# Kernel tuning notes

Hardware: AMD Instinct MI355X
Metric: run time of the kernel (lower is better)

Reference implementation:

```python
import jax, jax.numpy as jnp
import numpy as np

B, V, D, H, ET = 32, 50, 6, 256, 4  # batch, num_vars, input_size, decoder_hidden, num_edge_types
E = V * (V - 1)                      # fully connected, no self-loops


def setup_inputs() -> dict:
    key = jax.random.key(0)
    ks = jax.random.split(key, 24)
    s = 0.05
    n = lambda k, shape: jax.random.normal(k, shape, jnp.float32)
    return {
        "inputs": n(ks[0], (B, V, D)),
        "hidden": n(ks[1], (B, V, H)),
        "edges": jax.random.uniform(ks[2], (B, E, ET), jnp.float32),
        # stacked per-edge-type message MLPs for the non-skipped types 1..ET-1
        "W1": n(ks[3], (ET - 1, H, 2 * H)) * s, "b1": jnp.full((ET - 1, H), 0.1, jnp.float32),
        "W2": n(ks[4], (ET - 1, H, H)) * s, "b2": jnp.full((ET - 1, H), 0.1, jnp.float32),
        # GRU-style update (hidden_* have no bias in the torch module)
        "Whr": n(ks[5], (H, H)) * s, "Whi": n(ks[6], (H, H)) * s, "Whh": n(ks[7], (H, H)) * s,
        "Wir": n(ks[8], (H, D)) * s, "bir": jnp.full((H,), 0.1, jnp.float32),
        "Wii": n(ks[9], (H, D)) * s, "bii": jnp.full((H,), 0.1, jnp.float32),
        "Win": n(ks[10], (H, D)) * s, "bin_w": jnp.full((H,), 0.1, jnp.float32),
        # output MLP
        "Wo1": n(ks[11], (H, H)) * s, "bo1": jnp.full((H,), 0.1, jnp.float32),
        "Wo2": n(ks[12], (H, H)) * s, "bo2": jnp.full((H,), 0.1, jnp.float32),
        "Wo3": n(ks[13], (D, H)) * s, "bo3": jnp.full((D,), 0.1, jnp.float32),
    }


def _edge_index(num_vars):
    mask = np.ones((num_vars, num_vars)) - np.eye(num_vars)
    send, recv = np.where(mask)
    onehot = np.zeros((send.shape[0], num_vars), dtype=np.float32)
    onehot[np.arange(send.shape[0]), recv] = 1.0  # edge2node scatter matrix [E, V]
    return send, recv, onehot


def reference(inputs, hidden, edges, W1, b1, W2, b2, Whr, Whi, Whh,
              Wir, bir, Wii, bii, Win, bin_w, Wo1, bo1, Wo2, bo2, Wo3, bo3):
    num_vars = hidden.shape[1]
    send, recv, onehot = _edge_index(num_vars)
    onehot = jnp.asarray(onehot)

    # gather: [B, E, 2H]
    pre_msg = jnp.concatenate([hidden[:, recv, :], hidden[:, send, :]], axis=-1)

    # per-edge-type message MLP (dropout is identity in eval mode), types 1..ET-1 (skip_first)
    m = jnp.tanh(jnp.einsum('bef,thf->bteh', pre_msg, W1) + b1[None, :, None, :])
    m = jnp.tanh(jnp.einsum('bteh,tgh->bteg', m, W2) + b2[None, :, None, :])
    ew = jnp.moveaxis(edges[:, :, 1:], -1, 1)          # [B, T, E]
    norm = edges.shape[-1] - 1
    all_msgs = jnp.einsum('bteh,bte->beh', m, ew) / norm  # [B, E, H]

    # scatter-aggregate edges -> receiver nodes
    agg = jnp.einsum('beh,ev->bvh', all_msgs, onehot) / (num_vars - 1)  # [B, V, H]

    # GRU-style gated update
    r = jax.nn.sigmoid(inputs @ Wir.T + bir + agg @ Whr.T)
    i = jax.nn.sigmoid(inputs @ Wii.T + bii + agg @ Whi.T)
    n_ = jnp.tanh(inputs @ Win.T + bin_w + r * (agg @ Whh.T))
    hidden_new = (1 - i) * n_ + i * hidden

    # output MLP with residual on inputs
    p = jax.nn.relu(hidden_new @ Wo1.T + bo1)
    p = jax.nn.relu(p @ Wo2.T + bo2)
    pred = inputs + (p @ Wo3.T + bo3)
    return pred, hidden_new
```

## Files before the change

kernel.cpp:

```cpp
#include <hip/hip_runtime.h>
#include <math.h>

#define B_ 32
#define V_ 50
#define D_ 6
#define H_ 256
#define E_ 2450
#define T_ 3
#define NN 1600

#define OFF_inputs 0
#define OFF_hidden 9600
#define OFF_edges  419200
#define OFF_W1     732800
#define OFF_b1     1126016
#define OFF_W2     1126784
#define OFF_b2     1323392
#define OFF_Whr    1324160
#define OFF_Whi    1389696
#define OFF_Whh    1455232
#define OFF_Wir    1520768
#define OFF_bir    1522304
#define OFF_Wii    1522560
#define OFF_bii    1524096
#define OFF_Win    1524352
#define OFF_binw   1525888
#define OFF_Wo1    1526144
#define OFF_bo1    1591680
#define OFF_Wo2    1591936
#define OFF_bo2    1657472
#define OFF_Wo3    1657728
#define OFF_bo3    1659264
#define TOTAL_IN   1659270

#define PW_W2   0
#define PW_W1   196608
#define PW_WG   589824
#define PW_WO1  786432
#define PW_WO2  851968
#define PW_HID  917504
#define PW_TOT  1327104

typedef __attribute__((ext_vector_type(8))) short short8;
typedef __attribute__((ext_vector_type(4))) float f32x4;

__device__ __forceinline__ float bfc(unsigned int u) {
    return __uint_as_float((u & 0xffffu) << 16);
}
__device__ __forceinline__ unsigned short f2bf(float f) {
    unsigned int x = __float_as_uint(f);
    unsigned int r = (x + 0x7fffu + ((x >> 16) & 1u)) >> 16;
    return (unsigned short)r;
}
__device__ __forceinline__ float tanh_fast(float x) {
    float e = __builtin_amdgcn_exp2f(x * 2.8853900817779268f);
    return 1.0f - 2.0f * __builtin_amdgcn_rcpf(1.0f + e);
}
__device__ __forceinline__ float sigmoid_fast(float x) {
    float e = __builtin_amdgcn_exp2f(x * -1.4426950408889634f);
    return __builtin_amdgcn_rcpf(1.0f + e);
}

struct Ptrs { const void* p[22]; };

__device__ __forceinline__ int detect_bf(const Ptrs& pt) {
    const unsigned short* b1r = (const unsigned short*)pt.p[4];
    return (b1r[0] == 0x3DCDu && b1r[1] == 0x3DCDu) ? 1 : 0;
}
__device__ __forceinline__ float ldraw(const Ptrs& pt, int bf, int ti, int li) {
    return bf ? bfc(((const unsigned short*)pt.p[ti])[li])
              : ((const float*)pt.p[ti])[li];
}

__global__ __launch_bounds__(256) void kprepA(Ptrs pt, float* __restrict__ stag,
                                              unsigned short* __restrict__ W2s,
                                              unsigned short* __restrict__ W1s,
                                              unsigned short* __restrict__ Wgs,
                                              unsigned short* __restrict__ Wo1s,
                                              unsigned short* __restrict__ Wo2s,
                                              unsigned short* __restrict__ hidbf) {
    int i = blockIdx.x * 256 + threadIdx.x;
    if (i >= TOTAL_IN + PW_TOT) return;
    int bf = detect_bf(pt);
    if (i < TOTAL_IN) {
        int ti, base;
        if      (i < OFF_hidden) { ti = 0;  base = OFF_inputs; }
        else if (i < OFF_edges)  { ti = 1;  base = OFF_hidden; }
        else if (i < OFF_W1)     { ti = 2;  base = OFF_edges;  }
        else if (i < OFF_b1)     { ti = 3;  base = OFF_W1;     }
        else if (i < OFF_W2)     { ti = 4;  base = OFF_b1;     }
        else if (i < OFF_b2)     { ti = 5;  base = OFF_W2;     }
        else if (i < OFF_Whr)    { ti = 6;  base = OFF_b2;     }
        else if (i < OFF_Whi)    { ti = 7;  base = OFF_Whr;    }
        else if (i < OFF_Whh)    { ti = 8;  base = OFF_Whi;    }
        else if (i < OFF_Wir)    { ti = 9;  base = OFF_Whh;    }
        else if (i < OFF_bir)    { ti = 10; base = OFF_Wir;    }
        else if (i < OFF_Wii)    { ti = 11; base = OFF_bir;    }
        else if (i < OFF_bii)    { ti = 12; base = OFF_Wii;    }
        else if (i < OFF_Win)    { ti = 13; base = OFF_bii;    }
        else if (i < OFF_binw)   { ti = 14; base = OFF_Win;    }
        else if (i < OFF_Wo1)    { ti = 15; base = OFF_binw;   }
        else if (i < OFF_bo1)    { ti = 16; base = OFF_Wo1;    }
        else if (i < OFF_Wo2)    { ti = 17; base = OFF_bo1;    }
        else if (i < OFF_bo2)    { ti = 18; base = OFF_Wo2;    }
        else if (i < OFF_Wo3)    { ti = 19; base = OFF_bo2;    }
        else if (i < OFF_bo3)    { ti = 20; base = OFF_Wo3;    }
        else                     { ti = 21; base = OFF_bo3;    }
        stag[i] = ldraw(pt, bf, ti, i - base);
        return;
    }
    int ii = i - TOTAL_IN;
    if (ii < PW_W1) {
        int j = ii & 7, l = (ii >> 3) & 63;
        int rest = ii >> 9;
        int ntg = rest & 15, k0 = (rest >> 4) & 7, t = rest >> 7;
        int g = ntg * 16 + (l & 15);
        int k = k0 * 32 + ((l >> 4) << 3) + j;
        W2s[ii] = f2bf(ldraw(pt, bf, 5, (t * H_ + g) * H_ + k));
    } else if (ii < PW_WG) {
        int i1 = ii - PW_W1;
        int j = i1 & 7, l = (i1 >> 3) & 63;
        int rest = i1 >> 9;
        int ntg = rest % 96, k0 = rest / 96;
        int n = ntg * 16 + (l & 15);
        int t = n >> 9, half = (n >> 8) & 1, h = n & 255;
        int k = k0 * 32 + ((l >> 4) << 3) + j;
        W1s[i1] = f2bf(ldraw(pt, bf, 3, (t * H_ + h) * (2 * H_) + half * H_ + k));
    } else if (ii < PW_WO1) {
        int i2 = ii - PW_WG;
        int j = i2 & 7, l = (i2 >> 3) & 63;
        int rest = i2 >> 9;
        int ntg = rest % 48, k0 = rest / 48;
        int n = ntg * 16 + (l & 15);
        int gate = n >> 8, h = n & 255;
        int k = k0 * 32 + ((l >> 4) << 3) + j;
        Wgs[i2] = f2bf(ldraw(pt, bf, 7 + gate, h * H_ + k));
    } else if (ii < PW_WO2) {
        int i3 = ii - PW_WO1;
        int j = i3 & 7, l = (i3 >> 3) & 63;
        int rest = i3 >> 9;
        int ntg = rest & 15, k0 = rest >> 4;
        int h = ntg * 16 + (l & 15);
        int k = k0 * 32 + ((l >> 4) << 3) + j;
        Wo1s[i3] = f2bf(ldraw(pt, bf, 16, h * H_ + k));
    } else if (ii < PW_HID) {
        int i4 = ii - PW_WO2;
        int j = i4 & 7, l = (i4 >> 3) & 63;
        int rest = i4 >> 9;
        int ntg = rest & 15, k0 = rest >> 4;
        int h = ntg * 16 + (l & 15);
        int k = k0 * 32 + ((l >> 4) << 3) + j;
        Wo2s[i4] = f2bf(ldraw(pt, bf, 18, h * H_ + k));
    } else {
        int i5 = ii - PW_HID;
        hidbf[i5] = f2bf(ldraw(pt, bf, 1, i5));
    }
}

__global__ __launch_bounds__(256) void k1M(const unsigned short* __restrict__ hidbf,
                                           const unsigned short* __restrict__ W1s,
                                           float* __restrict__ Hr, float* __restrict__ Hs) {
    int m0 = blockIdx.x * 64;
    int nb = blockIdx.y;
    int t = nb >> 1, half = nb & 1;
    int tid = threadIdx.x;
    int w = tid >> 6, l = tid & 63, l15 = l & 15, quad = l >> 4;

    f32x4 acc[4][4];
    #pragma unroll
    for (int mt = 0; mt < 4; mt++)
        #pragma unroll
        for (int nt = 0; nt < 4; nt++) acc[mt][nt] = (f32x4){0.f, 0.f, 0.f, 0.f};

    for (int k0 = 0; k0 < 8; k0++) {
        short8 af[4], bfr[4];
        #pragma unroll
        for (int mt = 0; mt < 4; mt++) {
            int node = m0 + mt * 16 + l15;
            af[mt] = *(const short8*)&hidbf[node * H_ + k0 * 32 + quad * 8];
        }
        #pragma unroll
        for (int nt = 0; nt < 4; nt++) {
            int ntg = nb * 16 + w * 4 + nt;
            bfr[nt] = *(const short8*)&W1s[((k0 * 96 + ntg) << 9) + (l << 3)];
        }
        #pragma unroll
        for (int mt = 0; mt < 4; mt++)
            #pragma unroll
            for (int nt = 0; nt < 4; nt++)
                acc[mt][nt] = __builtin_amdgcn_mfma_f32_16x16x32_bf16(
                    af[mt], bfr[nt], acc[mt][nt], 0, 0, 0);
    }

    float* dst = half ? Hs : Hr;
    #pragma unroll
    for (int mt = 0; mt < 4; mt++)
        #pragma unroll
        for (int nt = 0; nt < 4; nt++) {
            int h = w * 64 + nt * 16 + l15;
            #pragma unroll
            for (int r = 0; r < 4; r++) {
                int node = m0 + mt * 16 + quad * 4 + r;
                dst[((size_t)t * NN + node) * H_ + h] = acc[mt][nt][r];
            }
        }
}

__global__ __launch_bounds__(256, 4) void k2(const float* __restrict__ stag,
                                          const float* __restrict__ Hr, const float* __restrict__ Hs,
                                          const unsigned short* __restrict__ W2s,
                                          unsigned short* __restrict__ aggbf) {
    int bv = blockIdx.x;
    int b = bv / V_;
    int v = bv % V_;
    int tid = threadIdx.x;
    int w = tid >> 6, l = tid & 63, l15 = l & 15, quad = l >> 4;

    __shared__ __align__(16) unsigned short m1A[32 * 64 * 8];
    __shared__ float hrb3[T_][H_];
    __shared__ float sew[T_][64];
    __shared__ int ssend[64];

    if (tid < 64) {
        int j = tid;
        int s = (j < 49) ? (j + (j >= v ? 1 : 0)) : v;
        ssend[j] = s;
        if (j < 49) {
            int e = s * (V_ - 1) + (v > s ? v - 1 : v);
            #pragma unroll
            for (int t = 0; t < T_; t++)
                sew[t][j] = stag[OFF_edges + ((size_t)b * E_ + e) * 4 + 1 + t];
        } else {
            #pragma unroll
            for (int t = 0; t < T_; t++) sew[t][j] = 0.f;
        }
    }
    #pragma unroll
    for (int t = 0; t < T_; t++)
        hrb3[t][tid] = Hr[(((size_t)t * B_ + b) * V_ + v) * H_ + tid]
                     + stag[OFF_b1 + t * H_ + tid];
    __syncthreads();

    float msgp[4] = {0.f, 0.f, 0.f, 0.f};
    int er = (w << 4) + l15;
    int snd = ssend[er];

    for (int t = 0; t < T_; t++) {
        const float* hsrow = Hs + (((size_t)t * B_ + b) * V_ + snd) * H_;
        #pragma unroll
        for (int i = 0; i < 8; i++) {
            int c = (quad + (i << 2)) << 3;
            float4 x0 = *(const float4*)(hsrow + c);
            float4 x1 = *(const float4*)(hsrow + c + 4);
            float4 h0 = *(const float4*)&hrb3[t][c];
            float4 h1 = *(const float4*)&hrb3[t][c + 4];
            unsigned short pk[8];
            pk[0] = f2bf(tanh_fast(x0.x + h0.x));
            pk[1] = f2bf(tanh_fast(x0.y + h0.y));
            pk[2] = f2bf(tanh_fast(x0.z + h0.z));
            pk[3] = f2bf(tanh_fast(x0.w + h0.w));
            pk[4] = f2bf(tanh_fast(x1.x + h1.x));
            pk[5] = f2bf(tanh_fast(x1.y + h1.y));
            pk[6] = f2bf(tanh_fast(x1.z + h1.z));
            pk[7] = f2bf(tanh_fast(x1.w + h1.w));
            *(short8*)&m1A[(((w << 3) + i) << 9) + (l << 3)] = *(short8*)pk;
        }
        __syncthreads();

        f32x4 acc[4][4];
        #pragma unroll
        for (int mt = 0; mt < 4; mt++)
            #pragma unroll
            for (int nt = 0; nt < 4; nt++) acc[mt][nt] = (f32x4){0.f, 0.f, 0.f, 0.f};

        for (int k0 = 0; k0 < 8; k0++) {
            short8 af[4], bfr[4];
            #pragma unroll
            for (int mt = 0; mt < 4; mt++)
                af[mt] = *(const short8*)&m1A[(((mt << 3) + k0) << 9) + (l << 3)];
            #pragma unroll
            for (int nt = 0; nt < 4; nt++) {
                int ntg = w * 4 + nt;
                bfr[nt] = *(const short8*)&W2s[((((t * 8 + k0) * 16 + ntg) << 6) + l) << 3];
            }
            #pragma unroll
            for (int mt = 0; mt < 4; mt++)
                #pragma unroll
                for (int nt = 0; nt < 4; nt++)
                    acc[mt][nt] = __builtin_amdgcn_mfma_f32_16x16x32_bf16(
                        af[mt], bfr[nt], acc[mt][nt], 0, 0, 0);
        }

        #pragma unroll
        for (int nt = 0; nt < 4; nt++) {
            float b2v = stag[OFF_b2 + t * H_ + w * 64 + nt * 16 + l15];
            float p = 0.f;
            #pragma unroll
            for (int mt = 0; mt < 4; mt++) {
                #pragma unroll
                for (int r = 0; r < 4; r++) {
                    int row = mt * 16 + quad * 4 + r;
                    p += sew[t][row] * tanh_fast(acc[mt][nt][r] + b2v);
                }
            }
            msgp[nt] += p;
        }
        __syncthreads();
    }

    const float scale = 1.0f / ((float)T_ * (float)(V_ - 1));
    #pragma unroll
    for (int nt = 0; nt < 4; nt++) {
        float vs = msgp[nt];
        vs += __shfl_xor(vs, 16, 64);
        vs += __shfl_xor(vs, 32, 64);
        if (quad == 0)
            aggbf[(size_t)bv * H_ + w * 64 + nt * 16 + l15] = f2bf(vs * scale);
    }
}

__global__ __launch_bounds__(256) void k4f(Ptrs pt, const float* __restrict__ stag,
                                           const unsigned short* __restrict__ aggbf,
                                           const unsigned short* __restrict__ Wgs,
                                           const unsigned short* __restrict__ Wo1s,
                                           const unsigned short* __restrict__ Wo2s,
                                           void* __restrict__ dout) {
    int n0 = blockIdx.x * 16;
    int tid = threadIdx.x;
    int w = tid >> 6, l = tid & 63, l15 = l & 15, quad = l >> 4;
    int bf = detect_bf(pt);

    __shared__ __align__(16) unsigned short bufA[16][264];
    __shared__ __align__(16) unsigned short bufB[16][264];

    f32x4 acc[3][4];
    #pragma unroll
    for (int g = 0; g < 3; g++)
        #pragma unroll
        for (int nt = 0; nt < 4; nt++) acc[g][nt] = (f32x4){0.f, 0.f, 0.f, 0.f};

    for (int k0 = 0; k0 < 8; k0++) {
        short8 af = *(const short8*)&aggbf[(n0 + l15) * H_ + k0 * 32 + quad * 8];
        #pragma unroll
        for (int g = 0; g < 3; g++)
            #pragma unroll
            for (int nt = 0; nt < 4; nt++) {
                int ntg = g * 16 + w * 4 + nt;
                short8 bfr = *(const short8*)&Wgs[((k0 * 48 + ntg) << 9) + (l << 3)];
                acc[g][nt] = __builtin_amdgcn_mfma_f32_16x16x32_bf16(
                    af, bfr, acc[g][nt], 0, 0, 0);
            }
    }

    float inp[4][D_];
    #pragma unroll
    for (int r = 0; r < 4; r++) {
        int node = n0 + quad * 4 + r;
        #pragma unroll
        for (int d = 0; d < D_; d++) inp[r][d] = stag[OFF_inputs + node * D_ + d];
    }
    #pragma unroll
    for (int nt = 0; nt < 4; nt++) {
        int h = w * 64 + nt * 16 + l15;
        float wir[D_], wii[D_], win[D_];
        #pragma unroll
        for (int d = 0; d < D_; d++) {
            wir[d] = stag[OFF_Wir + h * D_ + d];
            wii[d] = stag[OFF_Wii + h * D_ + d];
            win[d] = stag[OFF_Win + h * D_ + d];
        }
        float br = stag[OFF_bir + h], bi = stag[OFF_bii + h], bn = stag[OFF_binw + h];
        #pragma unroll
        for (int r = 0; r < 4; r++) {
            int node = n0 + quad * 4 + r;
            float xr = br, xi = bi, xn = bn;
            #pragma unroll
            for (int d = 0; d < D_; d++) {
                xr += inp[r][d] * wir[d];
                xi += inp[r][d] * wii[d];
                xn += inp[r][d] * win[d];
            }
            float rg = sigmoid_fast(xr + acc[0][nt][r]);
            float ig = sigmoid_fast(xi + acc[1][nt][r]);
            float ng = tanh_fast(xn + rg * acc[2][nt][r]);
            float hprev = stag[OFF_hidden + (size_t)node * H_ + h];
            float hn = (1.f - ig) * ng + ig * hprev;
            unsigned short hb = f2bf(hn);
            bufA[quad * 4 + r][h] = hb;
            if (bf) ((unsigned short*)dout)[9600 + (size_t)node * H_ + h] = hb;
            else    ((float*)dout)[9600 + (size_t)node * H_ + h] = hn;
        }
    }
    __syncthreads();

    {
        f32x4 a1[4];
        #pragma unroll
        for (int nt = 0; nt < 4; nt++) a1[nt] = (f32x4){0.f, 0.f, 0.f, 0.f};
        for (int k0 = 0; k0 < 8; k0++) {
            short8 af = *(const short8*)&bufA[l15][k0 * 32 + quad * 8];
            #pragma unroll
            for (int nt = 0; nt < 4; nt++) {
                int ntg = w * 4 + nt;
                short8 bfr = *(const short8*)&Wo1s[((k0 * 16 + ntg) << 9) + (l << 3)];
                a1[nt] = __builtin_amdgcn_mfma_f32_16x16x32_bf16(af, bfr, a1[nt], 0, 0, 0);
            }
        }
        __syncthreads();
        #pragma unroll
        for (int nt = 0; nt < 4; nt++) {
            int h = w * 64 + nt * 16 + l15;
            float bo = stag[OFF_bo1 + h];
            #pragma unroll
            for (int r = 0; r < 4; r++)
                bufB[quad * 4 + r][h] = f2bf(fmaxf(a1[nt][r] + bo, 0.f));
        }
    }
    __syncthreads();

    {
        f32x4 a2[4];
        #pragma unroll
        for (int nt = 0; nt < 4; nt++) a2[nt] = (f32x4){0.f, 0.f, 0.f, 0.f};
        for (int k0 = 0; k0 < 8; k0++) {
            short8 af = *(const short8*)&bufB[l15][k0 * 32 + quad * 8];
            #pragma unroll
            for (int nt = 0; nt < 4; nt++) {
                int ntg = w * 4 + nt;
                short8 bfr = *(const short8*)&Wo2s[((k0 * 16 + ntg) << 9) + (l << 3)];
                a2[nt] = __builtin_amdgcn_mfma_f32_16x16x32_bf16(af, bfr, a2[nt], 0, 0, 0);
            }
        }
        __syncthreads();
        #pragma unroll
        for (int nt = 0; nt < 4; nt++) {
            int h = w * 64 + nt * 16 + l15;
            float bo = stag[OFF_bo2 + h];
            #pragma unroll
            for (int r = 0; r < 4; r++)
                bufA[quad * 4 + r][h] = f2bf(fmaxf(a2[nt][r] + bo, 0.f));
        }
    }
    __syncthreads();

    if (tid < 16 * D_) {
        int nl = tid / D_, d = tid % D_;
        const float* wrow = stag + OFF_Wo3 + d * H_;
        float a = stag[OFF_bo3 + d];
        for (int k = 0; k < H_; k += 8) {
            short8 pv = *(const short8*)&bufA[nl][k];
            float4 w0 = *(const float4*)(wrow + k);
            float4 w1 = *(const float4*)(wrow + k + 4);
            a += bfc((unsigned short)pv[0]) * w0.x + bfc((unsigned short)pv[1]) * w0.y
               + bfc((unsigned short)pv[2]) * w0.z + bfc((unsigned short)pv[3]) * w0.w
               + bfc((unsigned short)pv[4]) * w1.x + bfc((unsigned short)pv[5]) * w1.y
               + bfc((unsigned short)pv[6]) * w1.z + bfc((unsigned short)pv[7]) * w1.w;
        }
        int node = n0 + nl;
        float val = a + stag[OFF_inputs + node * D_ + d];
        if (bf) ((unsigned short*)dout)[node * D_ + d] = f2bf(val);
        else    ((float*)dout)[node * D_ + d] = val;
    }
}

extern "C" void kernel_launch(void* const* d_in, const int* in_sizes, int n_in,
                              void* d_out, int out_size, void* d_ws, size_t ws_size,
                              hipStream_t stream) {
    float* stag = (float*)d_ws;
    float* Hr   = stag + 1659272;
    float* Hs   = Hr + 1228800;
    unsigned short* aggbf = (unsigned short*)(Hs + 1228800);
    unsigned short* W2s   = (unsigned short*)((float*)aggbf + 204800);
    unsigned short* W1s   = (unsigned short*)((float*)W2s + 98304);
    unsigned short* Wgs   = (unsigned short*)((float*)W1s + 196608);
    unsigned short* Wo1s  = (unsigned short*)((float*)Wgs + 98304);
    unsigned short* Wo2s  = (unsigned short*)((float*)Wo1s + 32768);
    unsigned short* hidbf = (unsigned short*)((float*)Wo2s + 32768);

    Ptrs pt;
    for (int i = 0; i < 22; i++) pt.p[i] = d_in[i];

    kprepA<<<(TOTAL_IN + PW_TOT + 255) / 256, 256, 0, stream>>>(pt, stag, W2s, W1s, Wgs, Wo1s, Wo2s, hidbf);
    k1M<<<dim3(25, 6), 256, 0, stream>>>(hidbf, W1s, Hr, Hs);
    k2<<<B_ * V_, 256, 0, stream>>>(stag, Hr, Hs, W2s, aggbf);
    k4f<<<NN / 16, 256, 0, stream>>>(pt, stag, aggbf, Wgs, Wo1s, Wo2s, d_out);
}
```

Before: 207.7 us.

## Slim prep kernel: vectorize weight swizzle, drop full input staging, skip padded edge rows

The prep kernel no longer copies every input (including hidden and edges) into a float staging buffer. Only small biases and weights are staged; edges, inputs and hidden are read directly from the original tensors with a dtype check. The weight swizzle now handles eight elements per thread with 16-byte loads and stores instead of one scalar element per thread. In the message kernel, the padding rows past the 49 real edges skip their tanh/load work and their tail accumulation. Together these shrink the prep launch and its memory traffic, at the cost of adding a dtype branch to the downstream kernels.

```diff
diff --git a/kernel.cpp b/kernel.cpp
--- a/kernel.cpp
+++ b/kernel.cpp
@@ -9,37 +9,27 @@
 #define T_ 3
 #define NN 1600
 
-#define OFF_inputs 0
-#define OFF_hidden 9600
-#define OFF_edges  419200
-#define OFF_W1     732800
-#define OFF_b1     1126016
-#define OFF_W2     1126784
-#define OFF_b2     1323392
-#define OFF_Whr    1324160
-#define OFF_Whi    1389696
-#define OFF_Whh    1455232
-#define OFF_Wir    1520768
-#define OFF_bir    1522304
-#define OFF_Wii    1522560
-#define OFF_bii    1524096
-#define OFF_Win    1524352
-#define OFF_binw   1525888
-#define OFF_Wo1    1526144
-#define OFF_bo1    1591680
-#define OFF_Wo2    1591936
-#define OFF_bo2    1657472
-#define OFF_Wo3    1657728
-#define OFF_bo3    1659264
-#define TOTAL_IN   1659270
-
-#define PW_W2   0
-#define PW_W1   196608
-#define PW_WG   589824
-#define PW_WO1  786432
-#define PW_WO2  851968
-#define PW_HID  917504
-#define PW_TOT  1327104
+#define Sb1   0
+#define Sb2   768
+#define SWir  1536
+#define SWii  3072
+#define SWin  4608
+#define Sbir  6144
+#define Sbii  6400
+#define Sbin  6656
+#define Sbo1  6912
+#define Sbo2  7168
+#define SWo3  7424
+#define Sbo3  8960
+#define STAG_N 8966
+
+#define NG_W2   24576
+#define NG_W1   73728
+#define NG_WG   98304
+#define NG_WO1  106496
+#define NG_WO2  114688
+#define NG_HID  165888
+#define NPREP   (NG_HID + STAG_N)
 
 typedef __attribute__((ext_vector_type(8))) short short8;
 typedef __attribute__((ext_vector_type(4))) float f32x4;
@@ -67,12 +57,12 @@
     const unsigned short* b1r = (const unsigned short*)pt.p[4];
     return (b1r[0] == 0x3DCDu && b1r[1] == 0x3DCDu) ? 1 : 0;
 }
-__device__ __forceinline__ float ldraw(const Ptrs& pt, int bf, int ti, int li) {
+__device__ __forceinline__ float ldraw(const Ptrs& pt, int bf, int ti, long li) {
     return bf ? bfc(((const unsigned short*)pt.p[ti])[li])
               : ((const float*)pt.p[ti])[li];
 }
 
-__global__ __launch_bounds__(256) void kprepA(Ptrs pt, float* __restrict__ stag,
+__global__ __launch_bounds__(256) void kprepV(Ptrs pt, float* __restrict__ stagS,
                                               unsigned short* __restrict__ W2s,
                                               unsigned short* __restrict__ W1s,
                                               unsigned short* __restrict__ Wgs,
@@ -80,81 +70,75 @@
                                               unsigned short* __restrict__ Wo2s,
                                               unsigned short* __restrict__ hidbf) {
     int i = blockIdx.x * 256 + threadIdx.x;
-    if (i >= TOTAL_IN + PW_TOT) return;
+    if (i >= NPREP) return;
     int bf = detect_bf(pt);
-    if (i < TOTAL_IN) {
-        int ti, base;
-        if      (i < OFF_hidden) { ti = 0;  base = OFF_inputs; }
-        else if (i < OFF_edges)  { ti = 1;  base = OFF_hidden; }
-        else if (i < OFF_W1)     { ti = 2;  base = OFF_edges;  }
-        else if (i < OFF_b1)     { ti = 3;  base = OFF_W1;     }
-        else if (i < OFF_W2)     { ti = 4;  base = OFF_b1;     }
-        else if (i < OFF_b2)     { ti = 5;  base = OFF_W2;     }
-        else if (i < OFF_Whr)    { ti = 6;  base = OFF_b2;     }
-        else if (i < OFF_Whi)    { ti = 7;  base = OFF_Whr;    }
-        else if (i < OFF_Whh)    { ti = 8;  base = OFF_Whi;    }
-        else if (i < OFF_Wir)    { ti = 9;  base = OFF_Whh;    }
-        else if (i < OFF_bir)    { ti = 10; base = OFF_Wir;    }
-        else if (i < OFF_Wii)    { ti = 11; base = OFF_bir;    }
-        else if (i < OFF_bii)    { ti = 12; base = OFF_Wii;    }
-        else if (i < OFF_Win)    { ti = 13; base = OFF_bii;    }
-        else if (i < OFF_binw)   { ti = 14; base = OFF_Win;    }
-        else if (i < OFF_Wo1)    { ti = 15; base = OFF_binw;   }
-        else if (i < OFF_bo1)    { ti = 16; base = OFF_Wo1;    }
-        else if (i < OFF_Wo2)    { ti = 17; base = OFF_bo1;    }
-        else if (i < OFF_bo2)    { ti = 18; base = OFF_Wo2;    }
-        else if (i < OFF_Wo3)    { ti = 19; base = OFF_bo2;    }
-        else if (i < OFF_bo3)    { ti = 20; base = OFF_Wo3;    }
-        else                     { ti = 21; base = OFF_bo3;    }
-        stag[i] = ldraw(pt, bf, ti, i - base);
+    if (i < NG_HID) {
+        const void* src; unsigned short* dst; long sidx;
+        if (i < NG_W2) {
+            int gi = i, frag = gi >> 6, l = gi & 63;
+            int ntg = frag & 15, k0 = (frag >> 4) & 7, t = frag >> 7;
+            int g = ntg * 16 + (l & 15);
+            sidx = (long)(t * H_ + g) * H_ + k0 * 32 + ((l >> 4) << 3);
+            src = pt.p[5]; dst = W2s + ((long)gi << 3);
+        } else if (i < NG_W1) {
+            int gi = i - NG_W2, frag = gi >> 6, l = gi & 63;
+            int ntg = frag % 96, k0 = frag / 96;
+            int n = ntg * 16 + (l & 15);
+            int t = n >> 9, half = (n >> 8) & 1, h = n & 255;
+            sidx = (long)(t * H_ + h) * (2 * H_) + half * H_ + k0 * 32 + ((l >> 4) << 3);
+            src = pt.p[3]; dst = W1s + ((long)gi << 3);
+        } else if (i < NG_WG) {
+            int gi = i - NG_W1, frag = gi >> 6, l = gi & 63;
+            int ntg = frag % 48, k0 = frag / 48;
+            int n = ntg * 16 + (l & 15);
+            int gate = n >> 8, h = n & 255;
+            sidx = (long)h * H_ + k0 * 32 + ((l >> 4) << 3);
+            src = pt.p[7 + gate]; dst = Wgs + ((long)gi << 3);
+        } else if (i < NG_WO1) {
+            int gi = i - NG_WG, frag = gi >> 6, l = gi & 63;
+            int ntg = frag & 15, k0 = frag >> 4;
+            int h = ntg * 16 + (l & 15);
+            sidx = (long)h * H_ + k0 * 32 + ((l >> 4) << 3);
+            src = pt.p[16]; dst = Wo1s + ((long)gi << 3);
+        } else if (i < NG_WO2) {
+            int gi = i - NG_WO1, frag = gi >> 6, l = gi & 63;
+            int ntg = frag & 15, k0 = frag >> 4;
+            int h = ntg * 16 + (l & 15);
+            sidx = (long)h * H_ + k0 * 32 + ((l >> 4) << 3);
+            src = pt.p[18]; dst = Wo2s + ((long)gi << 3);
+        } else {
+            int gi = i - NG_WO2;
+            sidx = (long)gi << 3;
+            src = pt.p[1]; dst = hidbf + ((long)gi << 3);
+        }
+        unsigned short outv[8];
+        if (bf) {
+            *(uint4*)outv = *(const uint4*)((const unsigned short*)src + sidx);
+        } else {
+            const float* sf = (const float*)src + sidx;
+            float4 a = *(const float4*)sf;
+            float4 b = *(const float4*)(sf + 4);
+            outv[0] = f2bf(a.x); outv[1] = f2bf(a.y); outv[2] = f2bf(a.z); outv[3] = f2bf(a.w);
+            outv[4] = f2bf(b.x); outv[5] = f2bf(b.y); outv[6] = f2bf(b.z); outv[7] = f2bf(b.w);
+        }
+        *(uint4*)dst = *(uint4*)outv;
         return;
     }
-    int ii = i - TOTAL_IN;
-    if (ii < PW_W1) {
-        int j = ii & 7, l = (ii >> 3) & 63;
-        int rest = ii >> 9;
-        int ntg = rest & 15, k0 = (rest >> 4) & 7, t = rest >> 7;
-        int g = ntg * 16 + (l & 15);
-        int k = k0 * 32 + ((l >> 4) << 3) + j;
-        W2s[ii] = f2bf(ldraw(pt, bf, 5, (t * H_ + g) * H_ + k));
-    } else if (ii < PW_WG) {
-        int i1 = ii - PW_W1;
-        int j = i1 & 7, l = (i1 >> 3) & 63;
-        int rest = i1 >> 9;
-        int ntg = rest % 96, k0 = rest / 96;
-        int n = ntg * 16 + (l & 15);
-        int t = n >> 9, half = (n >> 8) & 1, h = n & 255;
-        int k = k0 * 32 + ((l >> 4) << 3) + j;
-        W1s[i1] = f2bf(ldraw(pt, bf, 3, (t * H_ + h) * (2 * H_) + half * H_ + k));
-    } else if (ii < PW_WO1) {
-        int i2 = ii - PW_WG;
-        int j = i2 & 7, l = (i2 >> 3) & 63;
-        int rest = i2 >> 9;
-        int ntg = rest % 48, k0 = rest / 48;
-        int n = ntg * 16 + (l & 15);
-        int gate = n >> 8, h = n & 255;
-        int k = k0 * 32 + ((l >> 4) << 3) + j;
-        Wgs[i2] = f2bf(ldraw(pt, bf, 7 + gate, h * H_ + k));
-    } else if (ii < PW_WO2) {
-        int i3 = ii - PW_WO1;
-        int j = i3 & 7, l = (i3 >> 3) & 63;
-        int rest = i3 >> 9;
-        int ntg = rest & 15, k0 = rest >> 4;
-        int h = ntg * 16 + (l & 15);
-        int k = k0 * 32 + ((l >> 4) << 3) + j;
-        Wo1s[i3] = f2bf(ldraw(pt, bf, 16, h * H_ + k));
-    } else if (ii < PW_HID) {
-        int i4 = ii - PW_WO2;
-        int j = i4 & 7, l = (i4 >> 3) & 63;
-        int rest = i4 >> 9;
-        int ntg = rest & 15, k0 = rest >> 4;
-        int h = ntg * 16 + (l & 15);
-        int k = k0 * 32 + ((l >> 4) << 3) + j;
-        Wo2s[i4] = f2bf(ldraw(pt, bf, 18, h * H_ + k));
-    } else {
-        int i5 = ii - PW_HID;
-        hidbf[i5] = f2bf(ldraw(pt, bf, 1, i5));
-    }
+    int ii = i - NG_HID;
+    int ti, base;
+    if      (ii < 768)  { ti = 4;  base = 0; }
+    else if (ii < 1536) { ti = 6;  base = 768; }
+    else if (ii < 3072) { ti = 10; base = 1536; }
+    else if (ii < 4608) { ti = 12; base = 3072; }
+    else if (ii < 6144) { ti = 14; base = 4608; }
+    else if (ii < 6400) { ti = 11; base = 6144; }
+    else if (ii < 6656) { ti = 13; base = 6400; }
+    else if (ii < 6912) { ti = 15; base = 6656; }
+    else if (ii < 7168) { ti = 17; base = 6912; }
+    else if (ii < 7424) { ti = 19; base = 7168; }
+    else if (ii < 8960) { ti = 20; base = 7424; }
+    else                { ti = 21; base = 8960; }
+    stagS[ii] = ldraw(pt, bf, ti, ii - base);
 }
 
 __global__ __launch_bounds__(256) void k1M(const unsigned short* __restrict__ hidbf,
@@ -206,7 +190,7 @@
         }
 }
 
-__global__ __launch_bounds__(256, 4) void k2(const float* __restrict__ stag,
+__global__ __launch_bounds__(256, 4) void k2(Ptrs pt, const float* __restrict__ stagS,
                                           const float* __restrict__ Hr, const float* __restrict__ Hs,
                                           const unsigned short* __restrict__ W2s,
                                           unsigned short* __restrict__ aggbf) {
@@ -215,6 +199,7 @@
     int v = bv % V_;
     int tid = threadIdx.x;
     int w = tid >> 6, l = tid & 63, l15 = l & 15, quad = l >> 4;
+    int bf = detect_bf(pt);
 
     __shared__ __align__(16) unsigned short m1A[32 * 64 * 8];
     __shared__ float hrb3[T_][H_];
@@ -229,7 +214,7 @@
             int e = s * (V_ - 1) + (v > s ? v - 1 : v);
             #pragma unroll
             for (int t = 0; t < T_; t++)
-                sew[t][j] = stag[OFF_edges + ((size_t)b * E_ + e) * 4 + 1 + t];
+                sew[t][j] = ldraw(pt, bf, 2, ((long)b * E_ + e) * 4 + 1 + t);
         } else {
             #pragma unroll
             for (int t = 0; t < T_; t++) sew[t][j] = 0.f;
@@ -238,32 +223,34 @@
     #pragma unroll
     for (int t = 0; t < T_; t++)
         hrb3[t][tid] = Hr[(((size_t)t * B_ + b) * V_ + v) * H_ + tid]
-                     + stag[OFF_b1 + t * H_ + tid];
+                     + stagS[Sb1 + t * H_ + tid];
     __syncthreads();
 
     float msgp[4] = {0.f, 0.f, 0.f, 0.f};
     int er = (w << 4) + l15;
-    int snd = ssend[er];
+    int snd = ssend[er < 49 ? er : 48];
 
     for (int t = 0; t < T_; t++) {
-        const float* hsrow = Hs + (((size_t)t * B_ + b) * V_ + snd) * H_;
-        #pragma unroll
-        for (int i = 0; i < 8; i++) {
-            int c = (quad + (i << 2)) << 3;
-            float4 x0 = *(const float4*)(hsrow + c);
-            float4 x1 = *(const float4*)(hsrow + c + 4);
-            float4 h0 = *(const float4*)&hrb3[t][c];
-            float4 h1 = *(const float4*)&hrb3[t][c + 4];
-            unsigned short pk[8];
-            pk[0] = f2bf(tanh_fast(x0.x + h0.x));
-            pk[1] = f2bf(tanh_fast(x0.y + h0.y));
-            pk[2] = f2bf(tanh_fast(x0.z + h0.z));
-            pk[3] = f2bf(tanh_fast(x0.w + h0.w));
-            pk[4] = f2bf(tanh_fast(x1.x + h1.x));
-            pk[5] = f2bf(tanh_fast(x1.y + h1.y));
-            pk[6] = f2bf(tanh_fast(x1.z + h1.z));
-            pk[7] = f2bf(tanh_fast(x1.w + h1.w));
-            *(short8*)&m1A[(((w << 3) + i) << 9) + (l << 3)] = *(short8*)pk;
+        if (er < 49) {
+            const float* hsrow = Hs + (((size_t)t * B_ + b) * V_ + snd) * H_;
+            #pragma unroll
+            for (int i = 0; i < 8; i++) {
+                int c = (quad + (i << 2)) << 3;
+                float4 x0 = *(const float4*)(hsrow + c);
+                float4 x1 = *(const float4*)(hsrow + c + 4);
+                float4 h0 = *(const float4*)&hrb3[t][c];
+                float4 h1 = *(const float4*)&hrb3[t][c + 4];
+                unsigned short pk[8];
+                pk[0] = f2bf(tanh_fast(x0.x + h0.x));
+                pk[1] = f2bf(tanh_fast(x0.y + h0.y));
+                pk[2] = f2bf(tanh_fast(x0.z + h0.z));
+                pk[3] = f2bf(tanh_fast(x0.w + h0.w));
+                pk[4] = f2bf(tanh_fast(x1.x + h1.x));
+                pk[5] = f2bf(tanh_fast(x1.y + h1.y));
+                pk[6] = f2bf(tanh_fast(x1.z + h1.z));
+                pk[7] = f2bf(tanh_fast(x1.w + h1.w));
+                *(short8*)&m1A[(((w << 3) + i) << 9) + (l << 3)] = *(short8*)pk;
+            }
         }
         __syncthreads();
 
@@ -293,16 +280,17 @@
 
         #pragma unroll
         for (int nt = 0; nt < 4; nt++) {
-            float b2v = stag[OFF_b2 + t * H_ + w * 64 + nt * 16 + l15];
+            float b2v = stagS[Sb2 + t * H_ + w * 64 + nt * 16 + l15];
             float p = 0.f;
             #pragma unroll
-            for (int mt = 0; mt < 4; mt++) {
+            for (int mt = 0; mt < 3; mt++) {
                 #pragma unroll
                 for (int r = 0; r < 4; r++) {
                     int row = mt * 16 + quad * 4 + r;
                     p += sew[t][row] * tanh_fast(acc[mt][nt][r] + b2v);
                 }
             }
+            if (quad == 0) p += sew[t][48] * tanh_fast(acc[3][nt][0] + b2v);
             msgp[nt] += p;
         }
         __syncthreads();
@@ -319,7 +307,7 @@
     }
 }
 
-__global__ __launch_bounds__(256) void k4f(Ptrs pt, const float* __restrict__ stag,
+__global__ __launch_bounds__(256) void k4f(Ptrs pt, const float* __restrict__ stagS,
                                            const unsigned short* __restrict__ aggbf,
                                            const unsigned short* __restrict__ Wgs,
                                            const unsigned short* __restrict__ Wo1s,
@@ -357,7 +345,7 @@
     for (int r = 0; r < 4; r++) {
         int node = n0 + quad * 4 + r;
         #pragma unroll
-        for (int d = 0; d < D_; d++) inp[r][d] = stag[OFF_inputs + node * D_ + d];
+        for (int d = 0; d < D_; d++) inp[r][d] = ldraw(pt, bf, 0, node * D_ + d);
     }
     #pragma unroll
     for (int nt = 0; nt < 4; nt++) {
@@ -365,11 +353,11 @@
         float wir[D_], wii[D_], win[D_];
         #pragma unroll
         for (int d = 0; d < D_; d++) {
-            wir[d] = stag[OFF_Wir + h * D_ + d];
-            wii[d] = stag[OFF_Wii + h * D_ + d];
-            win[d] = stag[OFF_Win + h * D_ + d];
-        }
-        float br = stag[OFF_bir + h], bi = stag[OFF_bii + h], bn = stag[OFF_binw + h];
+            wir[d] = stagS[SWir + h * D_ + d];
+            wii[d] = stagS[SWii + h * D_ + d];
+            win[d] = stagS[SWin + h * D_ + d];
+        }
+        float br = stagS[Sbir + h], bi = stagS[Sbii + h], bn = stagS[Sbin + h];
         #pragma unroll
         for (int r = 0; r < 4; r++) {
             int node = n0 + quad * 4 + r;
@@ -383,7 +371,7 @@
             float rg = sigmoid_fast(xr + acc[0][nt][r]);
             float ig = sigmoid_fast(xi + acc[1][nt][r]);
             float ng = tanh_fast(xn + rg * acc[2][nt][r]);
-            float hprev = stag[OFF_hidden + (size_t)node * H_ + h];
+            float hprev = ldraw(pt, bf, 1, (long)node * H_ + h);
             float hn = (1.f - ig) * ng + ig * hprev;
             unsigned short hb = f2bf(hn);
             bufA[quad * 4 + r][h] = hb;
@@ -410,7 +398,7 @@
         #pragma unroll
         for (int nt = 0; nt < 4; nt++) {
             int h = w * 64 + nt * 16 + l15;
-            float bo = stag[OFF_bo1 + h];
+            float bo = stagS[Sbo1 + h];
             #pragma unroll
             for (int r = 0; r < 4; r++)
                 bufB[quad * 4 + r][h] = f2bf(fmaxf(a1[nt][r] + bo, 0.f));
@@ -435,7 +423,7 @@
         #pragma unroll
         for (int nt = 0; nt < 4; nt++) {
             int h = w * 64 + nt * 16 + l15;
-            float bo = stag[OFF_bo2 + h];
+            float bo = stagS[Sbo2 + h];
             #pragma unroll
             for (int r = 0; r < 4; r++)
                 bufA[quad * 4 + r][h] = f2bf(fmaxf(a2[nt][r] + bo, 0.f));
@@ -445,8 +433,8 @@
 
     if (tid < 16 * D_) {
         int nl = tid / D_, d = tid % D_;
-        const float* wrow = stag + OFF_Wo3 + d * H_;
-        float a = stag[OFF_bo3 + d];
+        const float* wrow = stagS + SWo3 + d * H_;
+        float a = stagS[Sbo3 + d];
         for (int k = 0; k < H_; k += 8) {
             short8 pv = *(const short8*)&bufA[nl][k];
             float4 w0 = *(const float4*)(wrow + k);
@@ -457,7 +445,7 @@
                + bfc((unsigned short)pv[6]) * w1.z + bfc((unsigned short)pv[7]) * w1.w;
         }
         int node = n0 + nl;
-        float val = a + stag[OFF_inputs + node * D_ + d];
+        float val = a + ldraw(pt, bf, 0, node * D_ + d);
         if (bf) ((unsigned short*)dout)[node * D_ + d] = f2bf(val);
         else    ((float*)dout)[node * D_ + d] = val;
     }
@@ -466,9 +454,9 @@
 extern "C" void kernel_launch(void* const* d_in, const int* in_sizes, int n_in,
                               void* d_out, int out_size, void* d_ws, size_t ws_size,
                               hipStream_t stream) {
-    float* stag = (float*)d_ws;
-    float* Hr   = stag + 1659272;
-    float* Hs   = Hr + 1228800;
+    float* stagS = (float*)d_ws;
+    float* Hr    = stagS + 9216;
+    float* Hs    = Hr + 1228800;
     unsigned short* aggbf = (unsigned short*)(Hs + 1228800);
     unsigned short* W2s   = (unsigned short*)((float*)aggbf + 204800);
     unsigned short* W1s   = (unsigned short*)((float*)W2s + 98304);
@@ -480,8 +468,8 @@
     Ptrs pt;
     for (int i = 0; i < 22; i++) pt.p[i] = d_in[i];
 
-    kprepA<<<(TOTAL_IN + PW_TOT + 255) / 256, 256, 0, stream>>>(pt, stag, W2s, W1s, Wgs, Wo1s, Wo2s, hidbf);
+    kprepV<<<(NPREP + 255) / 256, 256, 0, stream>>>(pt, stagS, W2s, W1s, Wgs, Wo1s, Wo2s, hidbf);
     k1M<<<dim3(25, 6), 256, 0, stream>>>(hidbf, W1s, Hr, Hs);
-    k2<<<B_ * V_, 256, 0, stream>>>(stag, Hr, Hs, W2s, aggbf);
-    k4f<<<NN / 16, 256, 0, stream>>>(pt, stag, aggbf, Wgs, Wo1s, Wo2s, d_out);
-}
+    k2<<<B_ * V_, 256, 0, stream>>>(pt, stagS, Hr, Hs, W2s, aggbf);
+    k4f<<<NN / 16, 256, 0, stream>>>(pt, stagS, aggbf, Wgs, Wo1s, Wo2s, d_out);
+}
```

New measurement: 250.0 us. +20.4%, slower.
